# Optimization experiments

Measured on AMD Instinct MI355X. Metric: run time of the kernel, lower is better.

Reference implementation:

```python
import jax, jax.numpy as jnp
import numpy as np
from jax.scipy.special import digamma

BETA = 0.1      # init kwarg beta
HIST_K = 4      # init kwarg history_len (KSG embedding / history length)
KNN_K = 3       # number of nearest neighbors in the KSG estimator


def _cheb_dist(u):
    """Pairwise Chebyshev (max-norm) distances for u: [M, d] -> [M, M].
    Scans over feature columns to avoid materializing an [M, M, d] tensor."""
    M = u.shape[0]
    def body(carry, col):  # col: [M]
        return jnp.maximum(carry, jnp.abs(col[:, None] - col[None, :])), None
    d0 = jnp.zeros((M, M), u.dtype)
    d, _ = jax.lax.scan(body, d0, u.T)
    return d


def _transfer_entropy(src, tgt):
    """KSG (Kraskov) transfer entropy TE(src -> tgt) with history HIST_K.
    src, tgt: [N, D] multivariate series (N samples along axis 0).
    TE = I(tgt_t ; src_{t-1..t-k} | tgt_{t-1..t-k}) via kNN/digamma CMI."""
    N = src.shape[0]
    M = N - HIST_K  # usable samples after embedding

    def past(a):  # stacked k-history embedding: [M, HIST_K * D]
        return jnp.concatenate(
            [a[HIST_K - l: HIST_K - l + M] for l in range(1, HIST_K + 1)], axis=1)

    A = tgt[HIST_K:]      # future target  [M, D]
    Bp = past(src)        # source history [M, k*D]
    Cp = past(tgt)        # target history [M, k*D]

    dA, dB, dC = _cheb_dist(A), _cheb_dist(Bp), _cheb_dist(Cp)
    dAC = jnp.maximum(dA, dC)   # (future, tgt-past) subspace
    dBC = jnp.maximum(dB, dC)   # (src-past, tgt-past) subspace
    dJ = jnp.maximum(dAC, dB)   # full joint space

    eye = jnp.eye(M, dtype=bool)
    dJ_noself = jnp.where(eye, jnp.inf, dJ)
    # eps_i = distance to the KNN_K-th nearest neighbor in the joint space
    eps = -jax.lax.top_k(-dJ_noself, KNN_K)[0][:, -1]  # [M]

    def count(d):  # strict-ball neighbor counts, excluding self
        return jnp.sum((d < eps[:, None]) & ~eye, axis=1).astype(jnp.float32)

    nAC, nBC, nC = count(dAC), count(dBC), count(dC)
    psi_k = digamma(jnp.asarray(KNN_K, jnp.float32))
    return psi_k + jnp.mean(digamma(nC + 1.0) - digamma(nAC + 1.0) - digamma(nBC + 1.0))


def setup_inputs() -> dict:
    key = jax.random.key(0)
    x = jax.random.normal(key, (1024, 8, 4, 8), dtype=jnp.float32)  # [B, T, V, D]
    return {"x": x}


def reference(x):
    B, T, V, D = x.shape
    scale = BETA * (1.0 / (T * V * D))
    var = jnp.transpose(x, (2, 1, 0, 3))              # [V, T, B, D]
    ys = var[:, 0]                                    # [V, B, D] target series
    P = V * (T - 1)
    xs = var[:, 1:].reshape(P, B, D)                  # all source series
    ys_rep = jnp.broadcast_to(ys[:, None], (V, T - 1, B, D)).reshape(P, B, D)
    te = jax.vmap(_transfer_entropy)(xs, ys_rep)      # [P]
    aggs = te.reshape(V, T - 1).sum(axis=1)           # per-variate sum over j
    return scale * jnp.mean(aggs)
```

## Files before the change

### kernel.cpp

```cpp
#include <hip/hip_runtime.h>
#include <math.h>

constexpr int NB = 1024;
constexpr int NT = 8;
constexpr int NV = 4;
constexpr int ND = 8;
constexpr int M = NB - 4;
constexpr int NTASK = NV * (NT - 1);
constexpr int SEGSTEPS = 32;
constexpr int BLKY = 17;


__device__ __forceinline__ int swzS(int r) { return r ^ ((r >> 5) & 7); }
__device__ __forceinline__ int swzM(int r) { return r ^ ((r >> 5) & 31); }

__device__ __forceinline__ int Ufn(int g) {
  const unsigned long long pk = 0ULL | (13ULL << 6) | (24ULL << 12) | (33ULL << 18)
      | (40ULL << 24) | (45ULL << 30) | (48ULL << 36) | (49ULL << 42);
  int pref = (int)((pk >> (6 * (g & 7))) & 63);
  return (525 * g - g * g + g - 64 * (g >> 3) - pref) >> 4;
}

__device__ __forceinline__ float cheb8(const float4& a0, const float4& a1,
                                       const float4& b0, const float4& b1) {
  float m0 = fmaxf(fabsf(a0.x - b0.x), fabsf(a0.y - b0.y));
  float m1 = fmaxf(fabsf(a0.z - b0.z), fabsf(a0.w - b0.w));
  float m2 = fmaxf(fabsf(a1.x - b1.x), fabsf(a1.y - b1.y));
  float m3 = fmaxf(fabsf(a1.z - b1.z), fabsf(a1.w - b1.w));
  return fmaxf(fmaxf(m0, m1), fmaxf(m2, m3));
}

template <typename P>
__device__ __forceinline__ void cas3(P* a, unsigned v) {
  unsigned o = atomicMin(a + 0, v); v = v > o ? v : o;
  o = atomicMin(a + 1, v);          v = v > o ? v : o;
  atomicMin(a + 2, v);
}

__global__ void k_init(double* psi, unsigned* eps3, unsigned* counts, double* accum) {
  int gid = blockIdx.x * 256 + threadIdx.x;
  int stride = gridDim.x * 256;
  for (int j = gid; j < NTASK * 1020 * 3; j += stride) eps3[j] = 0xFFFFFFFFu;
  for (int j = gid; j < NTASK * 1020; j += stride) counts[j] = 0u;
  if (gid == 0) *accum = 0.0;
  if (gid >= 1 && gid < NB) {
    double x = (double)gid, acc = 0.0;
    while (x < 10.0) { acc -= 1.0 / x; x += 1.0; }
    double inv = 1.0 / x, i2 = inv * inv;
    double ps = log(x) - 0.5 * inv
              - i2 * (1.0 / 12.0 - i2 * (1.0 / 120.0 - i2 * (1.0 / 252.0)));
    psi[gid] = ps + acc;
  }
}

template <int PASS>
__global__ __launch_bounds__(256, 2)
void k_pass(const float* __restrict__ x, unsigned* __restrict__ eps3,
            unsigned* __restrict__ counts) {
  extern __shared__ char ldsraw[];
  float4* S4 = (float4*)ldsraw;
  unsigned* M3 = (unsigned*)(ldsraw + 65536);
  float* EPSF = (float*)(ldsraw + 65536);
  unsigned* CNT = (unsigned*)(ldsraw + 65536 + 4096);

  const int task = blockIdx.x;
  const int v = task / (NT - 1), ts = 1 + task % (NT - 1);
  const int tid = threadIdx.x;

  const float4* x4 = (const float4*)x;
  for (int idx = tid; idx < 2 * NB; idx += 256) {
    int ser = idx >> 10, row = idx & 1023;
    int t = ser ? ts : 0;
    int gb = ((row * NT + t) * NV + v) * 2;
    int slot = swzS(row);
    S4[ser * 2048 + slot] = x4[gb];
    S4[ser * 2048 + 1024 + slot] = x4[gb + 1];
  }
  if constexpr (PASS == 1) {
    for (int j = tid; j < 1024 * 3; j += 256) M3[j] = 0xFFFFFFFFu;
  } else {
    for (int r = tid; r < 1024; r += 256) {
      int row = swzM(r);
      float e = 0.0f;
      if (row < 1020) {
        const unsigned* g = eps3 + (task * 1020 + row) * 3;
        unsigned m = g[0]; unsigned m1 = g[1]; unsigned m2 = g[2];
        m = m > m1 ? m : m1; m = m > m2 ? m : m2;
        e = __uint_as_float(m);
      }
      EPSF[r] = e;
      CNT[r] = 0u;
    }
  }
  __syncthreads();

  const int u = blockIdx.y * 256 + tid;
  const int U255 = Ufn(255);
  if (u < U255) {
    int G = 0;
    #pragma unroll
    for (int b = 128; b; b >>= 1) {
      int t2 = G + b;
      if (t2 <= 255 && Ufn(t2) <= u) G = t2;
    }
    const int dbase = 4 * G + 1;
    const int LG = 1019 - 4 * G;
    const int k0 = (u - Ufn(G)) * SEGSTEPS;
    const int kend = min(k0 + SEGSTEPS, LG);
    const int kb0 = k0 - 4;

    float uk3[4], pwA[4], pwB[4], pwC[4], vk2[4], qwA[4], qwB[4];
    #pragma unroll
    for (int g = 0; g < 4; ++g) {
      uk3[g] = pwA[g] = pwB[g] = pwC[g] = 0.f;
      vk2[g] = qwA[g] = qwB[g] = 0.f;
    }
    float4 ft[4][2], fs[4][2], nt[2][2], ns[2][2];
    float ef[4];
    #pragma unroll
    for (int g = 0; g < 4; ++g) {
      int rt = min(k0 + dbase + g, 1023), st = swzS(rt);
      ft[(1 + g) & 3][0] = S4[st]; ft[(1 + g) & 3][1] = S4[1024 + st];
      int rs = min(max(k0 - 1 + dbase + g, 0), 1023), ss = swzS(rs);
      fs[g & 3][0] = S4[2048 + ss]; fs[g & 3][1] = S4[3072 + ss];
      if constexpr (PASS == 2) {
        int re = min(max(kb0 + dbase + g, 0), 1023);
        ef[(1 + g) & 3] = EPSF[swzM(re)];
      }
    }
    {
      int rt = min(k0, 1023), st = swzS(rt);
      nt[0][0] = S4[st]; nt[0][1] = S4[1024 + st];
      int rs = min(max(k0 - 1, 0), 1023), ss = swzS(rs);
      ns[0][0] = S4[2048 + ss]; ns[0][1] = S4[3072 + ss];
    }

    #pragma unroll 1
    for (int it = 0; it < 9; ++it) {
      #pragma unroll
      for (int phi = 0; phi < 4; ++phi) {
        const int kk = kb0 + it * 4 + phi;
        float u4[4], v3[4];
        u4[0] = cheb8(nt[phi & 1][0], nt[phi & 1][1],
                      ft[(phi + 1) & 3][0], ft[(phi + 1) & 3][1]);
        v3[0] = cheb8(ns[phi & 1][0], ns[phi & 1][1],
                      fs[phi & 3][0], fs[phi & 3][1]);
        {
          int r1 = min(kk + dbase + 8, 1023), s1 = swzS(r1);
          ft[(phi + 1) & 3][0] = S4[s1]; ft[(phi + 1) & 3][1] = S4[1024 + s1];
          int r2 = min(kk + dbase + 7, 1023), s2 = swzS(r2);
          fs[phi & 3][0] = S4[2048 + s2]; fs[phi & 3][1] = S4[3072 + s2];
          int r3 = min(kk + 5, 1023), s3 = swzS(r3);
          nt[(phi + 1) & 1][0] = S4[s3]; nt[(phi + 1) & 1][1] = S4[1024 + s3];
          int r4 = min(max(kk + 4, 0), 1023), s4 = swzS(r4);
          ns[(phi + 1) & 1][0] = S4[2048 + s4]; ns[(phi + 1) & 1][1] = S4[3072 + s4];
        }
        float efn = 0.f;
        if constexpr (PASS == 2)
          efn = EPSF[swzM(min(max(kk + dbase + 4, 0), 1023))];
        #pragma unroll
        for (int g = 1; g < 4; ++g) {
          u4[g] = cheb8(nt[phi & 1][0], nt[phi & 1][1],
                        ft[(phi + 1 + g) & 3][0], ft[(phi + 1 + g) & 3][1]);
          v3[g] = cheb8(ns[phi & 1][0], ns[phi & 1][1],
                        fs[(phi + g) & 3][0], fs[(phi + g) & 3][1]);
        }
        const bool vb = (kk >= k0) & (kk < kend);
        const int rN = max(kk, 0);
        const int mN = swzM(rN);
        float eN = 0.f;
        unsigned accN = 0;
        if constexpr (PASS == 2) eN = EPSF[mN];
        #pragma unroll
        for (int g = 0; g < 4; ++g) {
          float pw3 = fmaxf(uk3[g], u4[g]);
          float dC  = fmaxf(pwA[g], pwC[g]);
          float dAC = fmaxf(dC, u4[g]);
          float qw2 = fmaxf(vk2[g], v3[g]);
          float dB  = fmaxf(qwA[g], qw2);
          float dBC = fmaxf(dB, dC);
          float dJ  = fmaxf(dAC, dB);
          pwA[g] = pwB[g]; pwB[g] = pwC[g]; pwC[g] = pw3; uk3[g] = u4[g];
          qwA[g] = qwB[g]; qwB[g] = qw2; vk2[g] = v3[g];
          const bool mg = vb & (kk + dbase + g <= 1019);
          const int rF = min(max(kk + dbase + g, 0), 1019);
          const int mF = swzM(rF);
          if constexpr (PASS == 1) {
            unsigned dm = mg ? __float_as_uint(dJ) : 0xFFFFFFFFu;
            cas3(M3 + mN * 3, dm);
            cas3(M3 + mF * 3, dm);
          } else {
            float eF = ef[(phi + 1 + g) & 3];
            unsigned pN = (unsigned)(dAC < eN) | ((unsigned)(dBC < eN) << 10)
                        | ((unsigned)(dC < eN) << 20);
            unsigned pF = (unsigned)(dAC < eF) | ((unsigned)(dBC < eF) << 10)
                        | ((unsigned)(dC < eF) << 20);
            accN += mg ? pN : 0u;
            atomicAdd(&CNT[mF], mg ? pF : 0u);
          }
        }
        if constexpr (PASS == 2) {
          atomicAdd(&CNT[mN], accN);
          ef[(phi + 1) & 3] = efn;
        }
      }
    }
  }
  __syncthreads();

  if constexpr (PASS == 1) {
    for (int r = tid; r < 1024; r += 256) {
      int row = swzM(r);
      if (row < 1020) {
        unsigned* g = eps3 + (task * 1020 + row) * 3;
        #pragma unroll
        for (int sl = 0; sl < 3; ++sl) {
          unsigned vv = M3[r * 3 + sl];
          if (vv != 0xFFFFFFFFu) cas3(g, vv);
        }
      }
    }
  } else {
    for (int r = tid; r < 1024; r += 256) {
      int row = swzM(r);
      if (row < 1020) {
        unsigned vv = CNT[r];
        if (vv) atomicAdd(&counts[task * 1020 + row], vv);
      }
    }
  }
}

__global__ void k_sum(const unsigned* __restrict__ counts,
                      const double* __restrict__ psi, double* __restrict__ accum) {
  int gid = blockIdx.x * 256 + threadIdx.x;
  double term = 0.0;
  if (gid < NTASK * 1020) {
    unsigned p = counts[gid];
    int n0 = p & 1023, n1 = (p >> 10) & 1023, n2 = p >> 20;
    term = psi[n2 + 1] - psi[n0 + 1] - psi[n1 + 1];
  }
  #pragma unroll
  for (int off = 32; off > 0; off >>= 1) term += __shfl_down(term, off);
  if ((threadIdx.x & 63) == 0) atomicAdd(accum, term);
}

__global__ void k_fin(const double* __restrict__ psi, const double* __restrict__ accum,
                      float* __restrict__ out) {
  if (threadIdx.x == 0 && blockIdx.x == 0) {
    double total = (double)NTASK * psi[3] + accum[0] / (double)M;
    double scale = 0.1 / (double)(NT * NV * ND) / (double)NV;
    out[0] = (float)(scale * total);
  }
}

extern "C" void kernel_launch(void* const* d_in, const int* in_sizes, int n_in,
                              void* d_out, int out_size, void* d_ws, size_t ws_size,
                              hipStream_t stream) {
  const float* x = (const float*)d_in[0];
  double* psi = (double*)d_ws;
  double* accum = psi + 1024;
  unsigned* eps3 = (unsigned*)((char*)d_ws + 8200);
  unsigned* counts = eps3 + NTASK * 1020 * 3;
  float* out = (float*)d_out;

  (void)hipFuncSetAttribute(reinterpret_cast<const void*>(&k_pass<1>),
                            hipFuncAttributeMaxDynamicSharedMemorySize, 77824);
  (void)hipFuncSetAttribute(reinterpret_cast<const void*>(&k_pass<2>),
                            hipFuncAttributeMaxDynamicSharedMemorySize, 77824);

  hipLaunchKernelGGL(k_init, dim3(120), dim3(256), 0, stream, psi, eps3, counts, accum);
  hipLaunchKernelGGL(HIP_KERNEL_NAME(k_pass<1>), dim3(NTASK, BLKY), dim3(256), 77824,
                     stream, x, eps3, counts);
  hipLaunchKernelGGL(HIP_KERNEL_NAME(k_pass<2>), dim3(NTASK, BLKY), dim3(256), 77824,
                     stream, x, eps3, counts);
  hipLaunchKernelGGL(k_sum, dim3(112), dim3(256), 0, stream, counts, psi, accum);
  hipLaunchKernelGGL(k_fin, dim3(1), dim3(1), 0, stream, psi, accum, out);
}
```

Baseline: 131.1 us.

## Filter top-3 atomic inserts by threshold and merge partial eps via separate kernel

In pass 1, each candidate distance is now checked against the current third-smallest value in LDS before the CAS-based top-3 insert runs, so most atomic CAS loops are skipped. Pass 2 skips atomic adds whose contribution is zero. The global merge of per-block top-3 lists changes from CAS atomics to plain stores into a workspace buffer, followed by a new reduction kernel, when the workspace is large enough. The trade-offs are an extra kernel launch, extra global traffic, and threshold reads that may be stale but remain safe.

```diff
diff --git a/kernel.cpp b/kernel.cpp
--- a/kernel.cpp
+++ b/kernel.cpp
@@ -56,7 +56,7 @@
 template <int PASS>
 __global__ __launch_bounds__(256, 2)
 void k_pass(const float* __restrict__ x, unsigned* __restrict__ eps3,
-            unsigned* __restrict__ counts) {
+            unsigned* __restrict__ counts, unsigned* __restrict__ part) {
   extern __shared__ char ldsraw[];
   float4* S4 = (float4*)ldsraw;
   unsigned* M3 = (unsigned*)(ldsraw + 65536);
@@ -170,7 +170,9 @@
         const int mN = swzM(rN);
         float eN = 0.f;
         unsigned accN = 0;
+        unsigned thrN = 0u;
         if constexpr (PASS == 2) eN = EPSF[mN];
+        else thrN = M3[mN * 3 + 2];
         #pragma unroll
         for (int g = 0; g < 4; ++g) {
           float pw3 = fmaxf(uk3[g], u4[g]);
@@ -186,21 +188,29 @@
           const int rF = min(max(kk + dbase + g, 0), 1019);
           const int mF = swzM(rF);
           if constexpr (PASS == 1) {
-            unsigned dm = mg ? __float_as_uint(dJ) : 0xFFFFFFFFu;
-            cas3(M3 + mN * 3, dm);
-            cas3(M3 + mF * 3, dm);
+            if (mg) {
+              unsigned dm = __float_as_uint(dJ);
+              if (dm < thrN) {
+                cas3(M3 + mN * 3, dm);
+                thrN = M3[mN * 3 + 2];
+              }
+              unsigned thrF = M3[mF * 3 + 2];
+              if (dm < thrF) cas3(M3 + mF * 3, dm);
+            }
           } else {
-            float eF = ef[(phi + 1 + g) & 3];
-            unsigned pN = (unsigned)(dAC < eN) | ((unsigned)(dBC < eN) << 10)
-                        | ((unsigned)(dC < eN) << 20);
-            unsigned pF = (unsigned)(dAC < eF) | ((unsigned)(dBC < eF) << 10)
-                        | ((unsigned)(dC < eF) << 20);
-            accN += mg ? pN : 0u;
-            atomicAdd(&CNT[mF], mg ? pF : 0u);
+            if (mg) {
+              float eF = ef[(phi + 1 + g) & 3];
+              unsigned pN = (unsigned)(dAC < eN) | ((unsigned)(dBC < eN) << 10)
+                          | ((unsigned)(dC < eN) << 20);
+              unsigned pF = (unsigned)(dAC < eF) | ((unsigned)(dBC < eF) << 10)
+                          | ((unsigned)(dC < eF) << 20);
+              accN += pN;
+              if (pF) atomicAdd(&CNT[mF], pF);
+            }
           }
         }
         if constexpr (PASS == 2) {
-          atomicAdd(&CNT[mN], accN);
+          if (accN) atomicAdd(&CNT[mN], accN);
           ef[(phi + 1) & 3] = efn;
         }
       }
@@ -209,14 +219,25 @@
   __syncthreads();
 
   if constexpr (PASS == 1) {
-    for (int r = tid; r < 1024; r += 256) {
-      int row = swzM(r);
-      if (row < 1020) {
-        unsigned* g = eps3 + (task * 1020 + row) * 3;
-        #pragma unroll
-        for (int sl = 0; sl < 3; ++sl) {
-          unsigned vv = M3[r * 3 + sl];
-          if (vv != 0xFFFFFFFFu) cas3(g, vv);
+    if (part) {
+      for (int r = tid; r < 1024; r += 256) {
+        int row = swzM(r);
+        if (row < 1020) {
+          unsigned* p = part + ((size_t)(task * BLKY + blockIdx.y) * 1020 + row) * 3;
+          p[0] = M3[r * 3 + 0]; p[1] = M3[r * 3 + 1]; p[2] = M3[r * 3 + 2];
+        }
+      }
+    } else {
+      for (int r = tid; r < 1024; r += 256) {
+        int row = swzM(r);
+        if (row < 1020) {
+          unsigned* g = eps3 + (task * 1020 + row) * 3;
+          unsigned thr = g[2];
+          #pragma unroll
+          for (int sl = 0; sl < 3; ++sl) {
+            unsigned vv = M3[r * 3 + sl];
+            if (vv < thr) cas3(g, vv);
+          }
         }
       }
     }
@@ -229,6 +250,25 @@
       }
     }
   }
+}
+
+__global__ void k_emerge(const unsigned* __restrict__ part, unsigned* __restrict__ eps3) {
+  int gid = blockIdx.x * 256 + threadIdx.x;
+  if (gid >= NTASK * 1020) return;
+  int task = gid / 1020, row = gid - task * 1020;
+  unsigned m0 = 0xFFFFFFFFu, m1 = 0xFFFFFFFFu, m2 = 0xFFFFFFFFu;
+  for (int y = 0; y < BLKY; ++y) {
+    const unsigned* p = part + ((size_t)(task * BLKY + y) * 1020 + row) * 3;
+    #pragma unroll
+    for (int sl = 0; sl < 3; ++sl) {
+      unsigned vv = p[sl];
+      unsigned l0 = min(m0, vv), h0 = max(m0, vv); m0 = l0;
+      unsigned l1 = min(m1, h0), h1 = max(m1, h0); m1 = l1;
+      m2 = min(m2, h1);
+    }
+  }
+  unsigned* g = eps3 + (size_t)gid * 3;
+  g[0] = m0; g[1] = m1; g[2] = m2;
 }
 
 __global__ void k_sum(const unsigned* __restrict__ counts,
@@ -264,6 +304,11 @@
   unsigned* counts = eps3 + NTASK * 1020 * 3;
   float* out = (float*)d_out;
 
+  const size_t part_off = 465160;
+  const size_t part_bytes = (size_t)NTASK * BLKY * 1020 * 3 * 4;
+  unsigned* part = (ws_size >= part_off + part_bytes + 64)
+                 ? (unsigned*)((char*)d_ws + part_off) : nullptr;
+
   (void)hipFuncSetAttribute(reinterpret_cast<const void*>(&k_pass<1>),
                             hipFuncAttributeMaxDynamicSharedMemorySize, 77824);
   (void)hipFuncSetAttribute(reinterpret_cast<const void*>(&k_pass<2>),
@@ -271,9 +316,11 @@
 
   hipLaunchKernelGGL(k_init, dim3(120), dim3(256), 0, stream, psi, eps3, counts, accum);
   hipLaunchKernelGGL(HIP_KERNEL_NAME(k_pass<1>), dim3(NTASK, BLKY), dim3(256), 77824,
-                     stream, x, eps3, counts);
+                     stream, x, eps3, counts, part);
+  if (part)
+    hipLaunchKernelGGL(k_emerge, dim3(112), dim3(256), 0, stream, part, eps3);
   hipLaunchKernelGGL(HIP_KERNEL_NAME(k_pass<2>), dim3(NTASK, BLKY), dim3(256), 77824,
-                     stream, x, eps3, counts);
+                     stream, x, eps3, counts, part);
   hipLaunchKernelGGL(k_sum, dim3(112), dim3(256), 0, stream, counts, psi, accum);
   hipLaunchKernelGGL(k_fin, dim3(1), dim3(1), 0, stream, psi, accum, out);
 }
```

New measurement: 122.3 us. 6.7% less time.
